# Performance work log

Measured on AMD Instinct MI355X. Metric: run time of the kernel, lower is better.

Reference implementation:

```python
import jax, jax.numpy as jnp
import numpy as np

EPS = 1e-5

def _bn_relu(x, g, b, m, v):
    # inference batchnorm + relu, NCHW, fused affine
    scale = g * jax.lax.rsqrt(v + EPS)
    shift = b - m * scale
    return jnp.maximum(x * scale[None, :, None, None] + shift[None, :, None, None], 0.0)

def _conv1x1(x, w):
    # x: [B,C,H,W], w: [O,C]
    return jnp.einsum('bchw,oc->bohw', x, w)

def _xcorr_depthwise(search, kernel, padding=0):
    # search: [B,C,Hs,Ws], kernel: [B,C,Hk,Wk]; grouped conv, groups=B*C
    B, C, Hs, Ws = search.shape
    Hk, Wk = kernel.shape[2], kernel.shape[3]
    x = search.reshape(1, B * C, Hs, Ws)
    k = kernel.reshape(B * C, 1, Hk, Wk)
    out = jax.lax.conv_general_dilated(
        x, k, window_strides=(1, 1), padding=[(padding, padding), (padding, padding)],
        feature_group_count=B * C, dimension_numbers=('NCHW', 'OIHW', 'NCHW'))
    return out.reshape(B, C, out.shape[2], out.shape[3])

def setup_inputs():
    key = jax.random.key(0)
    ks = jax.random.split(key, 20)
    B, Cin, HID, COUT = 128, 256, 256, 20
    s = 1.0 / np.sqrt(Cin)
    inp = {
        'kernel': jax.random.normal(ks[0], (B, Cin, 7, 7), jnp.float32),
        'search': jax.random.normal(ks[1], (B, Cin, 31, 31), jnp.float32),
        # conv_kernel branch (1x1 conv weight stored as [O,C]) + BN stats
        'w_k': jax.random.normal(ks[2], (HID, Cin), jnp.float32) * s,
        'g_k': 1.0 + 0.1 * jax.random.normal(ks[3], (HID,), jnp.float32),
        'b_k': 0.1 * jax.random.normal(ks[4], (HID,), jnp.float32),
        'm_k': 0.1 * jax.random.normal(ks[5], (HID,), jnp.float32),
        'v_k': jax.random.uniform(ks[6], (HID,), jnp.float32, 0.5, 1.5),
        # conv_search branch
        'w_s': jax.random.normal(ks[7], (HID, Cin), jnp.float32) * s,
        'g_s': 1.0 + 0.1 * jax.random.normal(ks[8], (HID,), jnp.float32),
        'b_s': 0.1 * jax.random.normal(ks[9], (HID,), jnp.float32),
        'm_s': 0.1 * jax.random.normal(ks[10], (HID,), jnp.float32),
        'v_s': jax.random.uniform(ks[11], (HID,), jnp.float32, 0.5, 1.5),
        # head: conv1(1x1)+BN+ReLU, conv2(1x1, bias)
        'w_h1': jax.random.normal(ks[12], (HID, HID), jnp.float32) * (1.0 / np.sqrt(HID)),
        'g_h': 1.0 + 0.1 * jax.random.normal(ks[13], (HID,), jnp.float32),
        'b_h': 0.1 * jax.random.normal(ks[14], (HID,), jnp.float32),
        'm_h': 0.1 * jax.random.normal(ks[15], (HID,), jnp.float32),
        'v_h': jax.random.uniform(ks[16], (HID,), jnp.float32, 0.5, 1.5),
        'w_h2': jax.random.normal(ks[17], (COUT, HID), jnp.float32) * (1.0 / np.sqrt(HID)),
        'bias_h2': 0.1 * jax.random.normal(ks[18], (COUT,), jnp.float32),
    }
    return inp

def reference(kernel, search, w_k, g_k, b_k, m_k, v_k, w_s, g_s, b_s, m_s, v_s,
              w_h1, g_h, b_h, m_h, v_h, w_h2, bias_h2):
    k = _bn_relu(_conv1x1(kernel, w_k), g_k, b_k, m_k, v_k)   # [B,256,7,7]
    s = _bn_relu(_conv1x1(search, w_s), g_s, b_s, m_s, v_s)   # [B,256,31,31]
    feat = _xcorr_depthwise(s, k, padding=0)                  # [B,256,25,25]
    y = _bn_relu(_conv1x1(feat, w_h1), g_h, b_h, m_h, v_h)
    out = _conv1x1(y, w_h2) + bias_h2[None, :, None, None]    # [B,20,25,25]
    return out
```

## Files before the change

kernel.cpp:

```cpp
#include <hip/hip_runtime.h>
#include <hip/hip_fp16.h>

typedef _Float16 f16;
typedef __attribute__((ext_vector_type(8))) _Float16 f16x8;
typedef __attribute__((ext_vector_type(4))) _Float16 f16x4;
typedef __attribute__((ext_vector_type(2))) _Float16 f16x2;
typedef __attribute__((ext_vector_type(4))) float f32x4;

#define MFMA16(a, b, c) __builtin_amdgcn_mfma_f32_16x16x32_f16((a), (b), (c), 0, 0, 0)

#define OFF_WK   0u
#define OFF_WS   131072u
#define OFF_WH1  262144u
#define OFF_W2P  393216u
#define OFF_SH   409600u
#define OFF_S    412672u
#define OFF_KF   63392768u

__global__ __launch_bounds__(256) void prep_weights(
    const float* __restrict__ wk, const float* __restrict__ gk, const float* __restrict__ bk,
    const float* __restrict__ mk, const float* __restrict__ vk,
    const float* __restrict__ wsr, const float* __restrict__ gs, const float* __restrict__ bs,
    const float* __restrict__ ms, const float* __restrict__ vs,
    const float* __restrict__ wh1, const float* __restrict__ gh, const float* __restrict__ bh,
    const float* __restrict__ mh, const float* __restrict__ vh,
    const float* __restrict__ wh2,
    f16* __restrict__ wk16, f16* __restrict__ ws16, f16* __restrict__ wh116,
    f16* __restrict__ w2p, float* __restrict__ shifts) {
  int o = blockIdx.x;
  int t = threadIdx.x;
  float sck = gk[o] * rsqrtf(vk[o] + 1e-5f);
  float scs = gs[o] * rsqrtf(vs[o] + 1e-5f);
  float sch = gh[o] * rsqrtf(vh[o] + 1e-5f);
  int idx = o * 256 + t;
  wk16[idx]  = (f16)(wk[idx] * sck);
  ws16[idx]  = (f16)(wsr[idx] * scs);
  wh116[idx] = (f16)(wh1[idx] * sch);
  if (o < 32) w2p[idx] = (o < 20) ? (f16)wh2[idx] : (f16)0;
  if (t == 0) {
    shifts[o]       = bk[o] - mk[o] * sck;
    shifts[256 + o] = bs[o] - ms[o] * scs;
    shifts[512 + o] = bh[o] - mh[o] * sch;
  }
}

__device__ __forceinline__ int pi_row(int q, int r) {
  return (q ^ (r << 2)) + (r << 4);
}

template <int P>
__global__ __launch_bounds__(256) void conv_nchw(
    const float* __restrict__ X, const f16* __restrict__ W,
    const float* __restrict__ shift, f16* __restrict__ out) {
  const int C = 256;
  int n0 = blockIdx.x * 64;
  int t = threadIdx.x;
  int lane = t & 63, wave = t >> 6;
  int fm = lane & 15, kg = lane >> 4;

  __shared__ f16 Bs[2][64 * 40];

  int b0 = n0 / P, bp0 = n0 - b0 * P;
  bool safe = (bp0 + 64 <= P);

  int px = (t & 15) * 4;
  int cpr = (t >> 4) * 2;
  const float* xb = X + ((size_t)b0 * C) * P + bp0 + px;

  int ub[4], up[4];
  if (!safe) {
#pragma unroll
    for (int e = 0; e < 4; ++e) {
      int gn = n0 + px + e;
      ub[e] = gn / P;
      up[e] = gn - ub[e] * P;
    }
  }

  int wrow[4];
#pragma unroll
  for (int e = 0; e < 4; ++e) wrow[e] = pi_row(t & 15, e);
  int rrow[4];
#pragma unroll
  for (int nf = 0; nf < 4; ++nf) rrow[nf] = pi_row(nf * 4 + (fm >> 2), fm & 3);

  const f16* wp = W + (size_t)(wave * 64 + fm) * C + kg * 8;

  f32x4 rb[3][2];
#pragma unroll
  for (int s = 0; s < 3; ++s) {
    int cl = s * 32 + cpr;
    if (safe) {
      rb[s][0] = *(const f32x4*)(xb + (size_t)cl * P);
      rb[s][1] = *(const f32x4*)(xb + (size_t)(cl + 1) * P);
    } else {
#pragma unroll
      for (int e = 0; e < 4; ++e) {
        rb[s][0][e] = X[((size_t)ub[e] * C + cl) * P + up[e]];
        rb[s][1][e] = X[((size_t)ub[e] * C + cl + 1) * P + up[e]];
      }
    }
  }

  f32x4 acc[4][4] = {};
#pragma unroll
  for (int ci = 0; ci < 8; ++ci) {
    f16x8 a[4];
#pragma unroll
    for (int of = 0; of < 4; ++of)
      a[of] = *(const f16x8*)(wp + (size_t)of * 16 * C + ci * 32);

    f16* buf = Bs[ci & 1];
#pragma unroll
    for (int e = 0; e < 4; ++e) {
      f16x2 v;
      v[0] = (f16)rb[ci % 3][0][e];
      v[1] = (f16)rb[ci % 3][1][e];
      *(f16x2*)&buf[wrow[e] * 40 + cpr] = v;
    }
    if (ci + 3 < 8) {
      int cl = (ci + 3) * 32 + cpr;
      if (safe) {
        rb[ci % 3][0] = *(const f32x4*)(xb + (size_t)cl * P);
        rb[ci % 3][1] = *(const f32x4*)(xb + (size_t)(cl + 1) * P);
      } else {
#pragma unroll
        for (int e = 0; e < 4; ++e) {
          rb[ci % 3][0][e] = X[((size_t)ub[e] * C + cl) * P + up[e]];
          rb[ci % 3][1][e] = X[((size_t)ub[e] * C + cl + 1) * P + up[e]];
        }
      }
    }
    asm volatile("s_waitcnt lgkmcnt(0)" ::: "memory");
    __builtin_amdgcn_s_barrier();

    f16x8 b[4];
#pragma unroll
    for (int nf = 0; nf < 4; ++nf)
      b[nf] = *(const f16x8*)&buf[rrow[nf] * 40 + kg * 8];
#pragma unroll
    for (int of = 0; of < 4; ++of)
#pragma unroll
      for (int nf = 0; nf < 4; ++nf)
        acc[of][nf] = MFMA16(a[of], b[nf], acc[of][nf]);
  }

#pragma unroll
  for (int of = 0; of < 4; ++of) {
    int orow = wave * 64 + of * 16 + kg * 4;
    f32x4 sh = *(const f32x4*)(shift + orow);
#pragma unroll
    for (int nf = 0; nf < 4; ++nf) {
      int n = n0 + nf * 16 + fm;
      f16x4 st;
#pragma unroll
      for (int r = 0; r < 4; ++r)
        st[r] = (f16)fmaxf(acc[of][nf][r] + sh[r], 0.0f);
      *(f16x4*)(out + (size_t)n * C + orow) = st;
    }
  }
}

__global__ __launch_bounds__(256) void xcorr_head(
    const f16* __restrict__ S ,
    const f16* __restrict__ Kf ,
    const f16* __restrict__ W1, const float* __restrict__ shift,
    const f16* __restrict__ W2p, const float* __restrict__ bias,
    float* __restrict__ out ) {
  const int C = 256;
  int id = blockIdx.x;
  int x = id & 7;
  int r = id >> 3;
  int g = r % 7;
  int b = (r / 7) * 8 + x;

  int t = threadIdx.x;
  int w = t >> 6, lane = t & 63;
  int fm = lane & 15, kg = lane >> 4;
  int oi = g * 4 + w;

  __shared__ char F[112 * 512];

  if (oi < 25) {
    const f16* Sb = S + (size_t)b * 961 * 256 + lane * 4;
    const f16* Kb = Kf + (size_t)b * 49 * 256 + lane * 4;
    f16x4 acc[25] = {};
    for (int di = 0; di < 7; ++di) {
      const f16* sp = Sb + (size_t)(oi + di) * 31 * 256;
      f16x4 srow[31];
#pragma unroll
      for (int j = 0; j < 31; ++j) srow[j] = *(const f16x4*)(sp + (size_t)j * 256);
      const f16* kp = Kb + (size_t)di * 7 * 256;
      f16x4 krow[7];
#pragma unroll
      for (int j = 0; j < 7; ++j) krow[j] = *(const f16x4*)(kp + (size_t)j * 256);
#pragma unroll
      for (int dj = 0; dj < 7; ++dj) {
        f16x4 kv = krow[dj];
#pragma unroll
        for (int oj = 0; oj < 25; ++oj)
          acc[oj] += srow[oj + dj] * kv;
      }
    }
#pragma unroll
    for (int oj = 0; oj < 25; ++oj) {
      int n = w * 25 + oj;
      *(f16x4*)(F + ((n * 512 + lane * 8) ^ ((n & 7) << 4))) = acc[oj];
    }
  } else {
    f16x4 z = {};
#pragma unroll
    for (int oj = 0; oj < 25; ++oj) {
      int n = w * 25 + oj;
      *(f16x4*)(F + ((n * 512 + lane * 8) ^ ((n & 7) << 4))) = z;
    }
  }
  __syncthreads();

  const f16* wp = W1 + (size_t)(w * 64 + fm) * C + kg * 8;
  f32x4 acc1[4][7] = {};
#pragma unroll
  for (int ci = 0; ci < 8; ++ci) {
    f16x8 a[4];
#pragma unroll
    for (int of = 0; of < 4; ++of)
      a[of] = *(const f16x8*)(wp + (size_t)of * 16 * C + ci * 32);
    f16x8 bf[7];
#pragma unroll
    for (int nf = 0; nf < 7; ++nf) {
      int n = nf * 16 + fm;
      bf[nf] = *(const f16x8*)(F + ((n * 512 + (ci * 32 + kg * 8) * 2) ^ ((n & 7) << 4)));
    }
#pragma unroll
    for (int of = 0; of < 4; ++of)
#pragma unroll
      for (int nf = 0; nf < 7; ++nf)
        acc1[of][nf] = MFMA16(a[of], bf[nf], acc1[of][nf]);
  }
  __syncthreads();

#pragma unroll
  for (int of = 0; of < 4; ++of) {
    int orow = w * 64 + of * 16 + kg * 4;
    f32x4 sh = *(const f32x4*)(shift + orow);
#pragma unroll
    for (int nf = 0; nf < 7; ++nf) {
      int n = nf * 16 + fm;
      f16x4 st;
#pragma unroll
      for (int q = 0; q < 4; ++q)
        st[q] = (f16)fmaxf(acc1[of][nf][q] + sh[q], 0.0f);
      *(f16x4*)(F + ((n * 512 + orow * 2) ^ ((n & 7) << 4))) = st;
    }
  }
  __syncthreads();

  f32x4 acc2[2][2] = {};
  int nfa = w, nfb = w + 4;
#pragma unroll
  for (int ci = 0; ci < 8; ++ci) {
    f16x8 a0 = *(const f16x8*)(W2p + (size_t)fm * C + ci * 32 + kg * 8);
    f16x8 a1 = *(const f16x8*)(W2p + (size_t)(16 + fm) * C + ci * 32 + kg * 8);
    int na = nfa * 16 + fm;
    f16x8 b0 = *(const f16x8*)(F + ((na * 512 + (ci * 32 + kg * 8) * 2) ^ ((na & 7) << 4)));
    acc2[0][0] = MFMA16(a0, b0, acc2[0][0]);
    acc2[1][0] = MFMA16(a1, b0, acc2[1][0]);
    if (nfb < 7) {
      int nb = nfb * 16 + fm;
      f16x8 b1 = *(const f16x8*)(F + ((nb * 512 + (ci * 32 + kg * 8) * 2) ^ ((nb & 7) << 4)));
      acc2[0][1] = MFMA16(a0, b1, acc2[0][1]);
      acc2[1][1] = MFMA16(a1, b1, acc2[1][1]);
    }
  }

#pragma unroll
  for (int q = 0; q < 2; ++q) {
    int nf = q ? nfb : nfa;
    if (nf >= 7) continue;
    int n = nf * 16 + fm;
    if (n < 100) {
      int oi2 = g * 4 + n / 25;
      int oj2 = n % 25;
      if (oi2 < 25) {
        float* op = out + (size_t)b * 12500 + oi2 * 25 + oj2;
#pragma unroll
        for (int of = 0; of < 2; ++of)
#pragma unroll
          for (int e = 0; e < 4; ++e) {
            int o = of * 16 + kg * 4 + e;
            if (o < 20) op[(size_t)o * 625] = acc2[of][q][e] + bias[o];
          }
      }
    }
  }
}

extern "C" void kernel_launch(void* const* d_in, const int* in_sizes, int n_in,
                              void* d_out, int out_size, void* d_ws, size_t ws_size,
                              hipStream_t stream) {
  const float* kernel_in = (const float*)d_in[0];
  const float* search    = (const float*)d_in[1];
  const float* w_k = (const float*)d_in[2];
  const float* g_k = (const float*)d_in[3];
  const float* b_k = (const float*)d_in[4];
  const float* m_k = (const float*)d_in[5];
  const float* v_k = (const float*)d_in[6];
  const float* w_s = (const float*)d_in[7];
  const float* g_s = (const float*)d_in[8];
  const float* b_s = (const float*)d_in[9];
  const float* m_s = (const float*)d_in[10];
  const float* v_s = (const float*)d_in[11];
  const float* w_h1 = (const float*)d_in[12];
  const float* g_h = (const float*)d_in[13];
  const float* b_h = (const float*)d_in[14];
  const float* m_h = (const float*)d_in[15];
  const float* v_h = (const float*)d_in[16];
  const float* w_h2 = (const float*)d_in[17];
  const float* bias_h2 = (const float*)d_in[18];
  float* out = (float*)d_out;

  char* ws = (char*)d_ws;
  f16* wk16  = (f16*)(ws + OFF_WK);
  f16* ws16  = (f16*)(ws + OFF_WS);
  f16* wh116 = (f16*)(ws + OFF_WH1);
  f16* w2p   = (f16*)(ws + OFF_W2P);
  float* shifts = (float*)(ws + OFF_SH);
  f16* sbuf = (f16*)(ws + OFF_S);
  f16* kbuf = (f16*)(ws + OFF_KF);

  prep_weights<<<256, 256, 0, stream>>>(w_k, g_k, b_k, m_k, v_k,
                                        w_s, g_s, b_s, m_s, v_s,
                                        w_h1, g_h, b_h, m_h, v_h, w_h2,
                                        wk16, ws16, wh116, w2p, shifts);

  conv_nchw<961><<<dim3(1922), 256, 0, stream>>>(search, ws16, shifts + 256, sbuf);
  conv_nchw<49><<<dim3(98), 256, 0, stream>>>(kernel_in, wk16, shifts + 0, kbuf);

  xcorr_head<<<dim3(896), 256, 0, stream>>>(
      sbuf, kbuf, wh116, shifts + 512, w2p, bias_h2, out);
}
```

Measured before the change: 163.7 us.

## Use per-image 128-pixel tiles for search conv and shrink head LDS buffer

Replaces the search-branch 1x1 conv with a new 512-thread kernel that tiles 128 pixels per block, one batch image per group of 8 blocks. Each block spans 256 output channels across 8 waves and uses a triple-buffered register prefetch of input channels. The last tile overlaps the previous one instead of crossing batch boundaries, so some pixels are computed twice but the partial-tile path goes away. Separately, the xcorr_head shared buffer shrinks from 112 to 100 rows by aliasing padded rows back onto valid ones, which cuts LDS use and may raise occupancy.

```diff
diff --git a/kernel.cpp b/kernel.cpp
--- a/kernel.cpp
+++ b/kernel.cpp
@@ -47,6 +47,96 @@
 __device__ __forceinline__ int pi_row(int q, int r) {
   return (q ^ (r << 2)) + (r << 4);
 }
+__device__ __forceinline__ int row128(int n) {
+  return (n & 64) + pi_row((n >> 2) & 15, n & 3);
+}
+
+__global__ __launch_bounds__(512) void conv_nchw128(
+    const float* __restrict__ X, const f16* __restrict__ W,
+    const float* __restrict__ shift, f16* __restrict__ out) {
+  const int C = 256, P = 961;
+  int b = blockIdx.x >> 3;
+  int ti = blockIdx.x & 7;
+  int n0 = ti * 128; if (n0 > P - 128) n0 = P - 128;
+  int t = threadIdx.x;
+  int w = t >> 6, lane = t & 63;
+  int fm = lane & 15, kg = lane >> 4;
+  int wo = (w & 3) * 64;
+  int wpx = (w >> 2) * 64;
+
+  __shared__ f16 Bs[2][128 * 40];
+
+  int px = (t & 31) * 4;
+  int cpr = (t >> 5) * 2;
+  const float* xb = X + ((size_t)b * C) * P + n0 + px;
+
+  int wrow[4];
+#pragma unroll
+  for (int e = 0; e < 4; ++e) wrow[e] = row128(px + e);
+  int rrow[4];
+#pragma unroll
+  for (int nf = 0; nf < 4; ++nf) rrow[nf] = row128(wpx + nf * 16 + fm);
+
+  const f16* wp = W + (size_t)(wo + fm) * C + kg * 8;
+
+  f32x4 rb[3][2];
+#pragma unroll
+  for (int s = 0; s < 3; ++s) {
+    int cl = s * 32 + cpr;
+    rb[s][0] = *(const f32x4*)(xb + (size_t)cl * P);
+    rb[s][1] = *(const f32x4*)(xb + (size_t)(cl + 1) * P);
+  }
+
+  f32x4 acc[4][4] = {};
+#pragma unroll
+  for (int ci = 0; ci < 8; ++ci) {
+    f16x8 a[4];
+#pragma unroll
+    for (int of = 0; of < 4; ++of)
+      a[of] = *(const f16x8*)(wp + (size_t)of * 16 * C + ci * 32);
+
+    f16* buf = Bs[ci & 1];
+#pragma unroll
+    for (int e = 0; e < 4; ++e) {
+      f16x2 v;
+      v[0] = (f16)rb[ci % 3][0][e];
+      v[1] = (f16)rb[ci % 3][1][e];
+      *(f16x2*)&buf[wrow[e] * 40 + cpr] = v;
+    }
+    if (ci + 3 < 8) {
+      int cl = (ci + 3) * 32 + cpr;
+      rb[ci % 3][0] = *(const f32x4*)(xb + (size_t)cl * P);
+      rb[ci % 3][1] = *(const f32x4*)(xb + (size_t)(cl + 1) * P);
+    }
+    asm volatile("s_waitcnt lgkmcnt(0)" ::: "memory");
+    __builtin_amdgcn_s_barrier();
+
+    f16x8 bfr[4];
+#pragma unroll
+    for (int nf = 0; nf < 4; ++nf)
+      bfr[nf] = *(const f16x8*)&buf[rrow[nf] * 40 + kg * 8];
+#pragma unroll
+    for (int of = 0; of < 4; ++of)
+#pragma unroll
+      for (int nf = 0; nf < 4; ++nf)
+        acc[of][nf] = MFMA16(a[of], bfr[nf], acc[of][nf]);
+  }
+
+#pragma unroll
+  for (int of = 0; of < 4; ++of) {
+    int orow = wo + of * 16 + kg * 4;
+    f32x4 sh = *(const f32x4*)(shift + orow);
+#pragma unroll
+    for (int nf = 0; nf < 4; ++nf) {
+      int n = n0 + wpx + nf * 16 + fm;
+      f16x4 st;
+#pragma unroll
+      for (int r = 0; r < 4; ++r)
+        st[r] = (f16)fmaxf(acc[of][nf][r] + sh[r], 0.0f);
+      *(f16x4*)(out + ((size_t)b * P + n) * C + orow) = st;
+    }
+  }
+}
 
 template <int P>
 __global__ __launch_bounds__(256) void conv_nchw(
@@ -179,7 +269,7 @@
   int fm = lane & 15, kg = lane >> 4;
   int oi = g * 4 + w;
 
-  __shared__ char F[112 * 512];
+  __shared__ char F[100 * 512];
 
   if (oi < 25) {
     const f16* Sb = S + (size_t)b * 961 * 256 + lane * 4;
@@ -229,7 +319,8 @@
 #pragma unroll
     for (int nf = 0; nf < 7; ++nf) {
       int n = nf * 16 + fm;
-      bf[nf] = *(const f16x8*)(F + ((n * 512 + (ci * 32 + kg * 8) * 2) ^ ((n & 7) << 4)));
+      int rn = n < 100 ? n : n - 100;
+      bf[nf] = *(const f16x8*)(F + ((rn * 512 + (ci * 32 + kg * 8) * 2) ^ ((rn & 7) << 4)));
     }
 #pragma unroll
     for (int of = 0; of < 4; ++of)
@@ -246,11 +337,13 @@
 #pragma unroll
     for (int nf = 0; nf < 7; ++nf) {
       int n = nf * 16 + fm;
-      f16x4 st;
-#pragma unroll
-      for (int q = 0; q < 4; ++q)
-        st[q] = (f16)fmaxf(acc1[of][nf][q] + sh[q], 0.0f);
-      *(f16x4*)(F + ((n * 512 + orow * 2) ^ ((n & 7) << 4))) = st;
+      if (n < 100) {
+        f16x4 st;
+#pragma unroll
+        for (int q = 0; q < 4; ++q)
+          st[q] = (f16)fmaxf(acc1[of][nf][q] + sh[q], 0.0f);
+        *(f16x4*)(F + ((n * 512 + orow * 2) ^ ((n & 7) << 4))) = st;
+      }
     }
   }
   __syncthreads();
@@ -267,7 +360,8 @@
     acc2[1][0] = MFMA16(a1, b0, acc2[1][0]);
     if (nfb < 7) {
       int nb = nfb * 16 + fm;
-      f16x8 b1 = *(const f16x8*)(F + ((nb * 512 + (ci * 32 + kg * 8) * 2) ^ ((nb & 7) << 4)));
+      int rnb = nb < 100 ? nb : nb - 100;
+      f16x8 b1 = *(const f16x8*)(F + ((rnb * 512 + (ci * 32 + kg * 8) * 2) ^ ((rnb & 7) << 4)));
       acc2[0][1] = MFMA16(a0, b1, acc2[0][1]);
       acc2[1][1] = MFMA16(a1, b1, acc2[1][1]);
     }
@@ -333,7 +427,7 @@
                                         w_h1, g_h, b_h, m_h, v_h, w_h2,
                                         wk16, ws16, wh116, w2p, shifts);
 
-  conv_nchw<961><<<dim3(1922), 256, 0, stream>>>(search, ws16, shifts + 256, sbuf);
+  conv_nchw128<<<dim3(1024), 512, 0, stream>>>(search, ws16, shifts + 256, sbuf);
   conv_nchw<49><<<dim3(98), 256, 0, stream>>>(kernel_in, wk16, shifts + 0, kbuf);
 
   xcorr_head<<<dim3(896), 256, 0, stream>>>(
```

Measured after the change: 163.1 us. About the same (-0.4%).
